# Performance work log

Measured on AMD Instinct MI355X. Metric: run time of the kernel, lower is better.

## Reference

```python
import jax, jax.numpy as jnp
import numpy as np

D_SVG, N_TYPE, N_PAR = 256, 10, 12          # deep-svg latent, animation types, animation params
PADDING_VALUE = -1.0
W_SVG, W_TYPE, W_PAR = 10.0, 0.1, 1.0       # weight_deep_svg, weight_type, weight_parameters

# ANIMATION_PARAMETER_INDICES as a dense boolean lookup: type t -> which params it uses
_pm = np.zeros((N_TYPE, N_PAR), dtype=bool)
for _t in range(N_TYPE):
    for _k in (_t % N_PAR, (_t + 1) % N_PAR, (_t + 2) % N_PAR):
        _pm[_t, _k] = True
PARAM_MASK = jnp.asarray(_pm)


def setup_inputs() -> dict:
    B, S = 256, 512
    F = D_SVG + N_TYPE + N_PAR
    key = jax.random.key(0)
    k1, k2, k3, k4, k5 = jax.random.split(key, 5)
    x = jax.random.normal(k1, (B, S, F), dtype=jnp.float32)
    cls = jax.random.randint(k2, (B, S), 0, N_TYPE)
    t_type = jax.nn.one_hot(cls, N_TYPE, dtype=jnp.float32)
    t_svg = jax.random.normal(k3, (B, S, D_SVG), dtype=jnp.float32)
    t_par = jax.random.normal(k4, (B, S, N_PAR), dtype=jnp.float32)
    target = jnp.concatenate([t_svg, t_type, t_par], axis=-1)
    # suffix-contiguous padding (matches the `break` semantics of the torch loop)
    lengths = jax.random.randint(k5, (B,), S // 2, S + 1)
    mask = jnp.arange(S)[None, :] >= lengths[:, None]            # True = padded
    target = jnp.where(mask[..., None], PADDING_VALUE, target)
    return {"input": x, "target": target, "target_padding_mask": mask}


def reference(input, target, target_padding_mask):
    # input[expanded_mask] = -100
    x = jnp.where(target_padding_mask[..., None], -100.0, input)
    in_svg, in_type, in_par = jnp.split(x, [D_SVG, D_SVG + N_TYPE], axis=-1)
    tg_svg, tg_type, tg_par = jnp.split(target, [D_SVG, D_SVG + N_TYPE], axis=-1)

    valid = tg_type[..., 0] != PADDING_VALUE                      # [B,S] non-padded rows
    t_idx = jnp.argmax(tg_type, axis=-1)                          # [B,S] animation type

    # vectorized replacement of the double for-loop: copy target params at the
    # type-dependent ANIMATION_PARAMETER_INDICES into input params
    pmask = PARAM_MASK[t_idx] & valid[..., None]                  # [B,S,N_PAR]
    in_par = jnp.where(pmask, tg_par, in_par)

    # CrossEntropyLoss(ignore_index=-1) over flattened type logits
    logits = in_type.reshape(-1, N_TYPE)
    labels = t_idx.reshape(-1)
    v = valid.reshape(-1).astype(logits.dtype)
    logp = jax.nn.log_softmax(logits, axis=-1)
    nll = -jnp.take_along_axis(logp, labels[:, None], axis=1)[:, 0]
    loss_type = jnp.sum(nll * v) / jnp.maximum(jnp.sum(v), 1.0)

    # plain MSE (mean over ALL elements, padding included, as in the original)
    loss_svg = jnp.mean((in_svg - tg_svg) ** 2)
    loss_par = jnp.mean((in_par - tg_par) ** 2)

    return W_SVG * loss_svg + W_TYPE * loss_type + W_PAR * loss_par
```

## Files before the change

### kernel.cpp

```cpp
#include <hip/hip_runtime.h>
#include <hip/hip_bf16.h>
#include <math.h>

#define D_SVG 256
#define N_TYPE 10
#define N_PAR 12
#define F_TOT (D_SVG + N_TYPE + N_PAR)
#define ROWS_PER_BLOCK 32
#define THREADS 256
#define N4_PER_BLOCK (ROWS_PER_BLOCK * F_TOT / 4)
#define FULL_ITERS (N4_PER_BLOCK / THREADS)
#define TAIL (N4_PER_BLOCK - FULL_ITERS * THREADS)


__global__ __launch_bounds__(THREADS) void meta_kernel(const float* __restrict__ input,
                                                       const float* __restrict__ target,
                                                       float4* __restrict__ part_a,
                                                       unsigned* __restrict__ bitmap) {
    __shared__ float sred[4][3];
    const int tid = threadIdx.x;
    const int r = blockIdx.x * THREADS + tid;

    const float2* __restrict__ tg2 = (const float2*)target;
    const float2* __restrict__ in2 = (const float2*)input;
    const long b2 = ((long)r * F_TOT + D_SVG) >> 1;

    float nll = 0.0f, cnt = 0.0f, corr = 0.0f;
    float2 t01 = tg2[b2];
    const bool valid = (t01.x != -1.0f);
    if (valid) {
        float tt[N_TYPE], l[N_TYPE];
        tt[0] = t01.x; tt[1] = t01.y;
        #pragma unroll
        for (int j = 1; j < 5; ++j) { float2 v = tg2[b2 + j]; tt[2*j] = v.x; tt[2*j+1] = v.y; }
        #pragma unroll
        for (int j = 0; j < 5; ++j) { float2 v = in2[b2 + j]; l[2*j] = v.x; l[2*j+1] = v.y; }
        int ti = 0; float best = tt[0];
        #pragma unroll
        for (int j = 1; j < N_TYPE; ++j) { if (tt[j] > best) { best = tt[j]; ti = j; } }
        float m = l[0];
        #pragma unroll
        for (int j = 1; j < N_TYPE; ++j) m = fmaxf(m, l[j]);
        float s = 0.0f;
        #pragma unroll
        for (int j = 0; j < N_TYPE; ++j) s += __expf(l[j] - m);
        nll = __logf(s) + m - l[ti];
        cnt = 1.0f;
        const long p = (long)r * F_TOT + (D_SVG + N_TYPE) + ti;
        float d0 = input[p]     - target[p];
        float d1 = input[p + 1] - target[p + 1];
        float d2 = input[p + 2] - target[p + 2];
        corr = d0 * d0 + d1 * d1 + d2 * d2;
    }

    unsigned long long bal = __ballot(valid);
    const int lane = tid & 63, wv = tid >> 6;
    if (lane == 0)  bitmap[blockIdx.x * 8 + wv * 2]     = (unsigned)bal;
    if (lane == 32) bitmap[blockIdx.x * 8 + wv * 2 + 1] = (unsigned)(bal >> 32);

    float vals[3] = {nll, cnt, corr};
    #pragma unroll
    for (int v = 0; v < 3; ++v) {
        float x = vals[v];
        #pragma unroll
        for (int off = 32; off > 0; off >>= 1) x += __shfl_down(x, off, 64);
        vals[v] = x;
    }
    if (lane == 0) {
        #pragma unroll
        for (int v = 0; v < 3; ++v) sred[wv][v] = vals[v];
    }
    __syncthreads();
    if (tid == 0) {
        float s0 = sred[0][0] + sred[1][0] + sred[2][0] + sred[3][0];
        float s1 = sred[0][1] + sred[1][1] + sred[2][1] + sred[3][1];
        float s2 = sred[0][2] + sred[1][2] + sred[2][2] + sred[3][2];
        part_a[blockIdx.x] = make_float4(s0, s1, s2, 0.0f);
    }
}

__global__ __launch_bounds__(THREADS) void bulk_kernel(const float* __restrict__ input,
                                                       const float* __restrict__ target,
                                                       const unsigned* __restrict__ bitmap,
                                                       float4* __restrict__ part_b) {
    __shared__ float sred[4][2];
    const int tid = threadIdx.x;
    const unsigned bits = bitmap[blockIdx.x];

    if (bits == 0u) {
        if (tid == 0) part_b[blockIdx.x] = make_float4(0.f, 0.f, 0.f, 0.f);
        return;
    }

    const long row0 = (long)blockIdx.x * ROWS_PER_BLOCK;
    const float4* __restrict__ in4p = (const float4*)(input + row0 * F_TOT);
    const float4* __restrict__ tg4p = (const float4*)(target + row0 * F_TOT);

    float svg_acc = 0.0f, par_acc = 0.0f;

    auto accum = [&](unsigned idx, float4 ivv, float4 tvv) {
        unsigned e0 = idx * 4u;
        unsigned ra = e0 / (unsigned)F_TOT;
        unsigned rb = (e0 + 2u) / (unsigned)F_TOT;
        unsigned fa = e0 - ra * (unsigned)F_TOT;
        unsigned fb = (e0 + 2u) - rb * (unsigned)F_TOT;
        unsigned vA = (bits >> ra) & 1u;
        unsigned vB = (bits >> rb) & 1u;
        float xs[4] = {ivv.x, ivv.y, ivv.z, ivv.w};
        float ts[4] = {tvv.x, tvv.y, tvv.z, tvv.w};
        #pragma unroll
        for (int j = 0; j < 4; ++j) {
            unsigned v    = (j < 2) ? vA : vB;
            unsigned feat = ((j < 2) ? fa : fb) + (unsigned)(j & 1);
            float d = xs[j] - ts[j];
            float sq = d * d;
            svg_acc += (v && feat < D_SVG) ? sq : 0.0f;
            par_acc += (v && feat >= D_SVG + N_TYPE) ? sq : 0.0f;
        }
    };

    float4 iv[FULL_ITERS], tv[FULL_ITERS];
    #pragma unroll
    for (int u = 0; u < FULL_ITERS; ++u) iv[u] = in4p[tid + u * THREADS];
    #pragma unroll
    for (int u = 0; u < FULL_ITERS; ++u) tv[u] = tg4p[tid + u * THREADS];
    #pragma unroll
    for (int u = 0; u < FULL_ITERS; ++u) accum(tid + u * THREADS, iv[u], tv[u]);
    if (tid < TAIL) {
        unsigned idx = FULL_ITERS * THREADS + tid;
        accum(idx, in4p[idx], tg4p[idx]);
    }

    float vals[2] = {svg_acc, par_acc};
    #pragma unroll
    for (int v = 0; v < 2; ++v) {
        float x = vals[v];
        #pragma unroll
        for (int off = 32; off > 0; off >>= 1) x += __shfl_down(x, off, 64);
        vals[v] = x;
    }
    const int wave = tid >> 6, lane = tid & 63;
    if (lane == 0) { sred[wave][0] = vals[0]; sred[wave][1] = vals[1]; }
    __syncthreads();
    if (tid == 0) {
        float s0 = sred[0][0] + sred[1][0] + sred[2][0] + sred[3][0];
        float s1 = sred[0][1] + sred[1][1] + sred[2][1] + sred[3][1];
        part_b[blockIdx.x] = make_float4(s0, s1, 0.0f, 0.0f);
    }
}

__global__ __launch_bounds__(256) void loss_final(const float4* __restrict__ part_b,
                                                  const float4* __restrict__ part_a,
                                                  float* __restrict__ out,
                                                  int nb, int na, int nrows) {
    __shared__ double sred[4][5];
    const int tid = threadIdx.x;
    double svg = 0.0, par = 0.0, nll = 0.0, cnt = 0.0, corr = 0.0;
    for (int i = tid; i < nb; i += 256) {
        float4 v = part_b[i];
        svg += v.x; par += v.y;
    }
    for (int i = tid; i < na; i += 256) {
        float4 v = part_a[i];
        nll += v.x; cnt += v.y; corr += v.z;
    }
    double vals[5] = {svg, par, nll, cnt, corr};
    #pragma unroll
    for (int v = 0; v < 5; ++v) {
        double x = vals[v];
        #pragma unroll
        for (int off = 32; off > 0; off >>= 1) x += __shfl_down(x, off, 64);
        vals[v] = x;
    }
    const int wave = tid >> 6, lane = tid & 63;
    if (lane == 0) {
        #pragma unroll
        for (int v = 0; v < 5; ++v) sred[wave][v] = vals[v];
    }
    __syncthreads();
    if (tid == 0) {
        double S[5];
        #pragma unroll
        for (int v = 0; v < 5; ++v)
            S[v] = sred[0][v] + sred[1][v] + sred[2][v] + sred[3][v];
        double npad = (double)nrows - S[3];
        double svg_t = S[0] + 9801.0 * D_SVG * npad;
        double par_t = S[1] - S[4] + 9801.0 * N_PAR * npad;
        double loss = 10.0 * svg_t / ((double)nrows * D_SVG)
                    + 0.1  * S[2] / fmax(S[3], 1.0)
                    + 1.0  * par_t / ((double)nrows * N_PAR);
        out[0] = (float)loss;
    }
}

extern "C" void kernel_launch(void* const* d_in, const int* in_sizes, int n_in,
                              void* d_out, int out_size, void* d_ws, size_t ws_size,
                              hipStream_t stream) {
    const float* input  = (const float*)d_in[0];
    const float* target = (const float*)d_in[1];
    float* out = (float*)d_out;

    const int nrows  = in_sizes[0] / F_TOT;
    const int blk_b  = nrows / ROWS_PER_BLOCK;
    const int blk_a  = nrows / THREADS;

    float4*   part_b = (float4*)d_ws;
    float4*   part_a = (float4*)((char*)d_ws + (size_t)blk_b * sizeof(float4));
    unsigned* bitmap = (unsigned*)((char*)part_a + (size_t)blk_a * sizeof(float4));

    meta_kernel<<<blk_a, THREADS, 0, stream>>>(input, target, part_a, bitmap);
    bulk_kernel<<<blk_b, THREADS, 0, stream>>>(input, target, bitmap, part_b);
    loss_final<<<1, 256, 0, stream>>>(part_b, part_a, out, blk_b, blk_a, nrows);
}
```

Before: 298.1 us.

## Fuse metadata and bulk kernels and trim loads to valid-prefix rows

Merges the type/CE metadata kernel into the bulk MSE kernel, so each 32-row block computes its own validity ballot, CE terms and the masked squared-error sums in one launch. This removes one kernel launch and the bitmap round trip through global memory. When the valid rows form a contiguous prefix, only the float4s covering those rows are loaded, which skips memory traffic for padded tails. The cost is a serial per-block validity load at the start and CE work done by only 32 threads per block.

```diff
diff --git a/kernel.cpp b/kernel.cpp
--- a/kernel.cpp
+++ b/kernel.cpp
@@ -1,5 +1,4 @@
 #include <hip/hip_runtime.h>
-#include <hip/hip_bf16.h>
 #include <math.h>
 
 #define D_SVG 256
@@ -9,32 +8,38 @@
 #define ROWS_PER_BLOCK 32
 #define THREADS 256
 #define N4_PER_BLOCK (ROWS_PER_BLOCK * F_TOT / 4)
-#define FULL_ITERS (N4_PER_BLOCK / THREADS)
-#define TAIL (N4_PER_BLOCK - FULL_ITERS * THREADS)
+#define N4_ITERS ((N4_PER_BLOCK + THREADS - 1) / THREADS)
 
 
-__global__ __launch_bounds__(THREADS) void meta_kernel(const float* __restrict__ input,
-                                                       const float* __restrict__ target,
-                                                       float4* __restrict__ part_a,
-                                                       unsigned* __restrict__ bitmap) {
-    __shared__ float sred[4][3];
-    const int tid = threadIdx.x;
-    const int r = blockIdx.x * THREADS + tid;
+__global__ __launch_bounds__(THREADS) void fused_kernel(const float* __restrict__ input,
+                                                        const float* __restrict__ target,
+                                                        float4* __restrict__ part,
+                                                        unsigned* __restrict__ bitmap) {
+    __shared__ float sred[4][4];
+    const int tid  = threadIdx.x;
+    const int lane = tid & 63, wave = tid >> 6;
+    const long row0 = (long)blockIdx.x * ROWS_PER_BLOCK;
 
-    const float2* __restrict__ tg2 = (const float2*)target;
-    const float2* __restrict__ in2 = (const float2*)input;
-    const long b2 = ((long)r * F_TOT + D_SVG) >> 1;
+    bool vld = false;
+    if (lane < 32) vld = (target[(row0 + lane) * F_TOT + D_SVG] != -1.0f);
+    const unsigned bits = (unsigned)__ballot(vld);
 
-    float nll = 0.0f, cnt = 0.0f, corr = 0.0f;
-    float2 t01 = tg2[b2];
-    const bool valid = (t01.x != -1.0f);
-    if (valid) {
+    if (bits == 0u) {
+        if (tid == 0) { part[blockIdx.x] = make_float4(0.f, 0.f, 0.f, 0.f);
+                        bitmap[blockIdx.x] = 0u; }
+        return;
+    }
+
+    float nll = 0.0f, corr = 0.0f;
+    if (tid < 32 && ((bits >> tid) & 1u)) {
+        const long rb = (row0 + tid) * F_TOT;
+        const float2* __restrict__ tg2 = (const float2*)(target + rb + D_SVG);
+        const float2* __restrict__ in2 = (const float2*)(input  + rb + D_SVG);
         float tt[N_TYPE], l[N_TYPE];
-        tt[0] = t01.x; tt[1] = t01.y;
         #pragma unroll
-        for (int j = 1; j < 5; ++j) { float2 v = tg2[b2 + j]; tt[2*j] = v.x; tt[2*j+1] = v.y; }
+        for (int j = 0; j < 5; ++j) { float2 v = tg2[j]; tt[2*j] = v.x; tt[2*j+1] = v.y; }
         #pragma unroll
-        for (int j = 0; j < 5; ++j) { float2 v = in2[b2 + j]; l[2*j] = v.x; l[2*j+1] = v.y; }
+        for (int j = 0; j < 5; ++j) { float2 v = in2[j]; l[2*j]  = v.x; l[2*j+1]  = v.y; }
         int ti = 0; float best = tt[0];
         #pragma unroll
         for (int j = 1; j < N_TYPE; ++j) { if (tt[j] > best) { best = tt[j]; ti = j; } }
@@ -45,58 +50,22 @@
         #pragma unroll
         for (int j = 0; j < N_TYPE; ++j) s += __expf(l[j] - m);
         nll = __logf(s) + m - l[ti];
-        cnt = 1.0f;
-        const long p = (long)r * F_TOT + (D_SVG + N_TYPE) + ti;
+        const long p = rb + (D_SVG + N_TYPE) + ti;
         float d0 = input[p]     - target[p];
         float d1 = input[p + 1] - target[p + 1];
         float d2 = input[p + 2] - target[p + 2];
         corr = d0 * d0 + d1 * d1 + d2 * d2;
     }
 
-    unsigned long long bal = __ballot(valid);
-    const int lane = tid & 63, wv = tid >> 6;
-    if (lane == 0)  bitmap[blockIdx.x * 8 + wv * 2]     = (unsigned)bal;
-    if (lane == 32) bitmap[blockIdx.x * 8 + wv * 2 + 1] = (unsigned)(bal >> 32);
+    const unsigned k   = (unsigned)__popc(bits);
+    const unsigned pre = (k == 32u) ? 0xffffffffu : ((1u << k) - 1u);
+    const unsigned n4v = (bits == pre) ? ((k * (unsigned)F_TOT + 3u) >> 2)
+                                       : (unsigned)N4_PER_BLOCK;
 
-    float vals[3] = {nll, cnt, corr};
-    #pragma unroll
-    for (int v = 0; v < 3; ++v) {
-        float x = vals[v];
-        #pragma unroll
-        for (int off = 32; off > 0; off >>= 1) x += __shfl_down(x, off, 64);
-        vals[v] = x;
-    }
-    if (lane == 0) {
-        #pragma unroll
-        for (int v = 0; v < 3; ++v) sred[wv][v] = vals[v];
-    }
-    __syncthreads();
-    if (tid == 0) {
-        float s0 = sred[0][0] + sred[1][0] + sred[2][0] + sred[3][0];
-        float s1 = sred[0][1] + sred[1][1] + sred[2][1] + sred[3][1];
-        float s2 = sred[0][2] + sred[1][2] + sred[2][2] + sred[3][2];
-        part_a[blockIdx.x] = make_float4(s0, s1, s2, 0.0f);
-    }
-}
-
-__global__ __launch_bounds__(THREADS) void bulk_kernel(const float* __restrict__ input,
-                                                       const float* __restrict__ target,
-                                                       const unsigned* __restrict__ bitmap,
-                                                       float4* __restrict__ part_b) {
-    __shared__ float sred[4][2];
-    const int tid = threadIdx.x;
-    const unsigned bits = bitmap[blockIdx.x];
-
-    if (bits == 0u) {
-        if (tid == 0) part_b[blockIdx.x] = make_float4(0.f, 0.f, 0.f, 0.f);
-        return;
-    }
-
-    const long row0 = (long)blockIdx.x * ROWS_PER_BLOCK;
-    const float4* __restrict__ in4p = (const float4*)(input + row0 * F_TOT);
+    const float4* __restrict__ in4p = (const float4*)(input  + row0 * F_TOT);
     const float4* __restrict__ tg4p = (const float4*)(target + row0 * F_TOT);
 
-    float svg_acc = 0.0f, par_acc = 0.0f;
+    float svg = 0.0f, par = 0.0f;
 
     auto accum = [&](unsigned idx, float4 ivv, float4 tvv) {
         unsigned e0 = idx * 4u;
@@ -114,57 +83,59 @@
             unsigned feat = ((j < 2) ? fa : fb) + (unsigned)(j & 1);
             float d = xs[j] - ts[j];
             float sq = d * d;
-            svg_acc += (v && feat < D_SVG) ? sq : 0.0f;
-            par_acc += (v && feat >= D_SVG + N_TYPE) ? sq : 0.0f;
+            svg += (v && feat < D_SVG) ? sq : 0.0f;
+            par += (v && feat >= D_SVG + N_TYPE) ? sq : 0.0f;
         }
     };
 
-    float4 iv[FULL_ITERS], tv[FULL_ITERS];
+    float4 iv[N4_ITERS], tv[N4_ITERS];
     #pragma unroll
-    for (int u = 0; u < FULL_ITERS; ++u) iv[u] = in4p[tid + u * THREADS];
+    for (int u = 0; u < N4_ITERS; ++u) {
+        unsigned idx = (unsigned)tid + u * THREADS;
+        if (idx < n4v) { iv[u] = in4p[idx]; tv[u] = tg4p[idx]; }
+    }
     #pragma unroll
-    for (int u = 0; u < FULL_ITERS; ++u) tv[u] = tg4p[tid + u * THREADS];
-    #pragma unroll
-    for (int u = 0; u < FULL_ITERS; ++u) accum(tid + u * THREADS, iv[u], tv[u]);
-    if (tid < TAIL) {
-        unsigned idx = FULL_ITERS * THREADS + tid;
-        accum(idx, in4p[idx], tg4p[idx]);
+    for (int u = 0; u < N4_ITERS; ++u) {
+        unsigned idx = (unsigned)tid + u * THREADS;
+        if (idx < n4v) accum(idx, iv[u], tv[u]);
     }
 
-    float vals[2] = {svg_acc, par_acc};
+    float vals[4] = {svg, par, nll, corr};
     #pragma unroll
-    for (int v = 0; v < 2; ++v) {
+    for (int v = 0; v < 4; ++v) {
         float x = vals[v];
         #pragma unroll
         for (int off = 32; off > 0; off >>= 1) x += __shfl_down(x, off, 64);
         vals[v] = x;
     }
-    const int wave = tid >> 6, lane = tid & 63;
-    if (lane == 0) { sred[wave][0] = vals[0]; sred[wave][1] = vals[1]; }
+    if (lane == 0) {
+        #pragma unroll
+        for (int v = 0; v < 4; ++v) sred[wave][v] = vals[v];
+    }
     __syncthreads();
     if (tid == 0) {
         float s0 = sred[0][0] + sred[1][0] + sred[2][0] + sred[3][0];
         float s1 = sred[0][1] + sred[1][1] + sred[2][1] + sred[3][1];
-        part_b[blockIdx.x] = make_float4(s0, s1, 0.0f, 0.0f);
+        float s2 = sred[0][2] + sred[1][2] + sred[2][2] + sred[3][2];
+        float s3 = sred[0][3] + sred[1][3] + sred[2][3] + sred[3][3];
+        part[blockIdx.x]   = make_float4(s0, s1, s2, s3);
+        bitmap[blockIdx.x] = bits;
     }
 }
 
-__global__ __launch_bounds__(256) void loss_final(const float4* __restrict__ part_b,
-                                                  const float4* __restrict__ part_a,
+__global__ __launch_bounds__(256) void loss_final(const float4* __restrict__ part,
+                                                  const unsigned* __restrict__ bitmap,
                                                   float* __restrict__ out,
-                                                  int nb, int na, int nrows) {
+                                                  int nb, int nrows) {
     __shared__ double sred[4][5];
     const int tid = threadIdx.x;
-    double svg = 0.0, par = 0.0, nll = 0.0, cnt = 0.0, corr = 0.0;
+    double svg = 0.0, par = 0.0, nll = 0.0, corr = 0.0, cnt = 0.0;
     for (int i = tid; i < nb; i += 256) {
-        float4 v = part_b[i];
-        svg += v.x; par += v.y;
+        float4 v = part[i];
+        svg += v.x; par += v.y; nll += v.z; corr += v.w;
+        cnt += (double)__popc(bitmap[i]);
     }
-    for (int i = tid; i < na; i += 256) {
-        float4 v = part_a[i];
-        nll += v.x; cnt += v.y; corr += v.z;
-    }
-    double vals[5] = {svg, par, nll, cnt, corr};
+    double vals[5] = {svg, par, nll, corr, cnt};
     #pragma unroll
     for (int v = 0; v < 5; ++v) {
         double x = vals[v];
@@ -183,11 +154,11 @@
         #pragma unroll
         for (int v = 0; v < 5; ++v)
             S[v] = sred[0][v] + sred[1][v] + sred[2][v] + sred[3][v];
-        double npad = (double)nrows - S[3];
+        double npad = (double)nrows - S[4];
         double svg_t = S[0] + 9801.0 * D_SVG * npad;
-        double par_t = S[1] - S[4] + 9801.0 * N_PAR * npad;
+        double par_t = S[1] - S[3] + 9801.0 * N_PAR * npad;
         double loss = 10.0 * svg_t / ((double)nrows * D_SVG)
-                    + 0.1  * S[2] / fmax(S[3], 1.0)
+                    + 0.1  * S[2] / fmax(S[4], 1.0)
                     + 1.0  * par_t / ((double)nrows * N_PAR);
         out[0] = (float)loss;
     }
@@ -200,15 +171,12 @@
     const float* target = (const float*)d_in[1];
     float* out = (float*)d_out;
 
-    const int nrows  = in_sizes[0] / F_TOT;
-    const int blk_b  = nrows / ROWS_PER_BLOCK;
-    const int blk_a  = nrows / THREADS;
+    const int nrows = in_sizes[0] / F_TOT;
+    const int blk   = nrows / ROWS_PER_BLOCK;
 
-    float4*   part_b = (float4*)d_ws;
-    float4*   part_a = (float4*)((char*)d_ws + (size_t)blk_b * sizeof(float4));
-    unsigned* bitmap = (unsigned*)((char*)part_a + (size_t)blk_a * sizeof(float4));
+    float4*   part   = (float4*)d_ws;
+    unsigned* bitmap = (unsigned*)((char*)d_ws + (size_t)blk * sizeof(float4));
 
-    meta_kernel<<<blk_a, THREADS, 0, stream>>>(input, target, part_a, bitmap);
-    bulk_kernel<<<blk_b, THREADS, 0, stream>>>(input, target, bitmap, part_b);
-    loss_final<<<1, 256, 0, stream>>>(part_b, part_a, out, blk_b, blk_a, nrows);
+    fused_kernel<<<blk, THREADS, 0, stream>>>(input, target, part, bitmap);
+    loss_final<<<1, 256, 0, stream>>>(part, bitmap, out, blk, nrows);
 }
```

Result: faster. 290.9 us (-2.4%).
